# Kernel optimization log

Hardware: AMD Instinct MI355X
Metric: run time of the kernel (lower is better)

## Reference

```python
import jax, jax.numpy as jnp
import numpy as np

N = 16384      # total nodes
E = 262144     # edges (avg degree 16)
HID = 1024     # hidden_dim
D = 768        # internal_dim
R = 6          # num_relations
B = 4          # num_bases
L = 2          # num_gnn_layers
BN_EPS = 1e-5
LN_EPS = 1e-5


def setup_inputs() -> dict:
    key = jax.random.key(0)
    ks = jax.random.split(key, 16)
    s = 0.02
    return {
        "h_text": jax.random.normal(ks[0], (N, HID), jnp.float32),
        "edge_index": jax.random.randint(ks[1], (2, E), 0, N, jnp.int32),
        "edge_type": jax.random.randint(ks[2], (E,), 0, R, jnp.int32),
        # input projection
        "w_in": jax.random.normal(ks[3], (HID, D), jnp.float32) * s,
        "b_in": jnp.zeros((D,), jnp.float32),
        # per-layer RGCN params (stacked over L layers)
        "basis": jax.random.normal(ks[4], (L, B, D, D), jnp.float32) * s,
        "comp": jax.random.normal(ks[5], (L, R, B), jnp.float32),
        "root": jax.random.normal(ks[6], (L, D, D), jnp.float32) * s,
        "conv_bias": jnp.zeros((L, D), jnp.float32),
        # per-layer BatchNorm affine params
        "bn_gamma": jnp.ones((L, D), jnp.float32),
        "bn_beta": jnp.zeros((L, D), jnp.float32),
        # output projection + LayerNorm
        "w_out": jax.random.normal(ks[7], (D, HID), jnp.float32) * s,
        "b_out": jnp.zeros((HID,), jnp.float32),
        "ln_gamma": jnp.ones((HID,), jnp.float32),
        "ln_beta": jnp.zeros((HID,), jnp.float32),
    }


def _rgcn_conv(x, src, dst, edge_type, basis, comp, root, bias):
    """PyG RGCNConv with basis decomposition, per-relation mean aggregation."""
    n = x.shape[0]
    # relation weights: W_r = sum_b comp[r,b] * basis[b]  -> [R, D, D]
    W = jnp.einsum('rb,bio->rio', comp, basis)
    # transform every node by every relation once: [R, N, D]
    h_all = jnp.einsum('ni,rio->rno', x, W)
    # per-(relation, target) in-degree for mean normalization
    counts = jnp.zeros((R, n), x.dtype).at[edge_type, dst].add(1.0)
    norm = 1.0 / counts[edge_type, dst]            # each indexed count >= 1
    msg = h_all[edge_type, src] * norm[:, None]    # [E, D] gathered messages
    agg = jax.ops.segment_sum(msg, dst, num_segments=n)
    return agg + x @ root + bias


def _batchnorm(x, gamma, beta):
    mean = jnp.mean(x, axis=0)
    var = jnp.var(x, axis=0)  # biased, as in torch BN training forward
    return gamma * (x - mean) * jax.lax.rsqrt(var + BN_EPS) + beta


def _layernorm(x, gamma, beta):
    mean = jnp.mean(x, axis=-1, keepdims=True)
    var = jnp.var(x, axis=-1, keepdims=True)
    return gamma * (x - mean) * jax.lax.rsqrt(var + LN_EPS) + beta


def reference(h_text, edge_index, edge_type, w_in, b_in, basis, comp, root,
              conv_bias, bn_gamma, bn_beta, w_out, b_out, ln_gamma, ln_beta):
    src, dst = edge_index[0], edge_index[1]
    x = jax.nn.relu(h_text @ w_in + b_in)
    for l in range(L):
        h_in = x
        x = _rgcn_conv(x, src, dst, edge_type, basis[l], comp[l], root[l], conv_bias[l])
        x = jax.nn.relu(x)
        x = x + h_in
        x = _batchnorm(x, bn_gamma[l], bn_beta[l])
    h_final = x @ w_out + b_out
    return _layernorm(h_final, ln_gamma, ln_beta)
```

## Files before the change

kernel.cpp:

```cpp
#include <hip/hip_runtime.h>
#include <hip/hip_bf16.h>

#define NN 16384
#define NE 262144
#define HIDD 1024
#define DD 768
#define RR 6
#define BB 4
#define LL 2
#define BN_EPS 1e-5f
#define LN_EPS 1e-5f

typedef __attribute__((ext_vector_type(8))) short bf16x8;
typedef __attribute__((ext_vector_type(4))) float f32x4;

__device__ __forceinline__ float b2f(unsigned short u) {
  union { unsigned int i; float f; } c;
  c.i = ((unsigned int)u) << 16;
  return c.f;
}
__device__ __forceinline__ unsigned short f2b(float f) {
  union { float f; unsigned int u; } c;
  c.f = f;
  unsigned int x = c.u;
  x += 0x7FFFu + ((x >> 16) & 1u);
  return (unsigned short)(x >> 16);
}

__device__ __forceinline__ void gll16(const unsigned short* g, unsigned short* l) {
  __builtin_amdgcn_global_load_lds(
      (const __attribute__((address_space(1))) unsigned int*)g,
      (__attribute__((address_space(3))) unsigned int*)l, 16, 0, 0);
}

__global__ void k_detect(const unsigned short* __restrict__ h, int* __restrict__ flag) {
  __shared__ int sh[256];
  int cnt = 0;
  for (int k = 0; k < 256; ++k) {
    ushort4 t = *(const ushort4*)&h[(size_t)(k * 256 + threadIdx.x) * 4];
    if ((t.x & 0x7F80) == 0x7F80) cnt++;
    if ((t.y & 0x7F80) == 0x7F80) cnt++;
    if ((t.z & 0x7F80) == 0x7F80) cnt++;
    if ((t.w & 0x7F80) == 0x7F80) cnt++;
  }
  sh[threadIdx.x] = cnt;
  __syncthreads();
  if (threadIdx.x == 0) {
    int t = 0;
    for (int i = 0; i < 256; ++i) t += sh[i];
    flag[0] = (t > 16) ? 1 : 0;
  }
}

template <int MODE>
__device__ __forceinline__ float load1t(const void* p, size_t i, int isf32) {
  if (MODE == 1 || (MODE == 0 && isf32)) return ((const float*)p)[i];
  return b2f(((const unsigned short*)p)[i]);
}

__global__ void k_cvt8(const void* s0, const void* s1, const void* s2, const void* s3,
                       const void* s4, const void* s5, const void* s6, const void* s7,
                       float* __restrict__ fpar, const int* __restrict__ flagp) {
  const int isf32 = flagp[0];
  const int seg = blockIdx.y;
  const int lens[8] = {768, 48, 1536, 1536, 1536, 1024, 1024, 1024};
  const int offs_[8] = {0, 768, 816, 2352, 3888, 5424, 6448, 7472};
  const void* srcs[8] = {s0, s1, s2, s3, s4, s5, s6, s7};
  int i = blockIdx.x * 256 + threadIdx.x;
  if (i < lens[seg]) fpar[offs_[seg] + i] = load1t<0>(srcs[seg], i, isf32);
}

__global__ void k_cvtb(const void* __restrict__ in, unsigned short* __restrict__ out,
                       int n, const int* __restrict__ flagp) {
  const int isf32 = flagp[0];
  int i = blockIdx.x * 256 + threadIdx.x;
  if (i < n) out[i] = f2b(load1t<0>(in, (size_t)i, isf32));
}

__global__ void k_fill(float* __restrict__ out, long n, float val) {
  long i = (long)blockIdx.x * 256 + threadIdx.x;
  if (i < n) out[i] = val;
}

__global__ __launch_bounds__(256) void k_transpose(const void* __restrict__ src,
                                                   long ioff,
                                                   unsigned short* __restrict__ dst,
                                                   int I, int J, int dstStride,
                                                   int dstOff,
                                                   const int* __restrict__ flagp) {
  const int isf32 = flagp[0];
  __shared__ unsigned short t[64][65];
  const int j0 = blockIdx.x * 64, i0 = blockIdx.y * 64;
  const int tx = threadIdx.x & 63, ty = threadIdx.x >> 6;
  for (int rr = ty; rr < 64; rr += 4)
    t[rr][tx] = f2b(load1t<0>(src, (size_t)ioff + (size_t)(i0 + rr) * J + j0 + tx, isf32));
  __syncthreads();
  for (int rr = ty; rr < 64; rr += 4)
    dst[(size_t)(j0 + rr) * dstStride + dstOff + i0 + tx] = t[tx][rr];
}

__global__ __launch_bounds__(256) void k_tbatch(const void* __restrict__ root, long roff,
                                                const void* __restrict__ basis, long boff,
                                                unsigned short* __restrict__ BT,
                                                const int* __restrict__ flagp) {
  const int isf32 = flagp[0];
  const int z = blockIdx.z;
  const void* src = (z == 0) ? root : basis;
  const long off = (z == 0) ? roff : boff + (long)(z - 1) * DD * DD;
  __shared__ unsigned short t[64][65];
  const int j0 = blockIdx.x * 64, i0 = blockIdx.y * 64;
  const int tx = threadIdx.x & 63, ty = threadIdx.x >> 6;
  for (int rr = ty; rr < 64; rr += 4)
    t[rr][tx] = f2b(load1t<0>(src, (size_t)off + (size_t)(i0 + rr) * DD + j0 + tx, isf32));
  __syncthreads();
  for (int rr = ty; rr < 64; rr += 4)
    BT[(size_t)(j0 + rr) * (5 * DD) + z * DD + i0 + tx] = t[tx][rr];
}

template <int BIAS, int RELU, int OUTB>
__global__ __launch_bounds__(256) void k_mgemm(const unsigned short* __restrict__ A,
                                               const unsigned short* __restrict__ Bt,
                                               const float* __restrict__ bias,
                                               void* __restrict__ C,
                                               int M, int Nn, int K) {
  __shared__ __align__(16) unsigned short Alds[2][128 * 32];
  __shared__ __align__(16) unsigned short Blds[2][128 * 32];
  const int tid = threadIdx.x;
  const int lane = tid & 63, w = tid >> 6;
  const int wm = w >> 1, wn = w & 1;
  const int fr = lane & 15, kg = lane >> 4;
  const int nwg = gridDim.x;
  int id = blockIdx.x;
  if ((nwg & 7) == 0) id = (id & 7) * (nwg >> 3) + (id >> 3);
  const int gx = Nn >> 7;
  const int m0 = (id / gx) * 128, n0 = (id % gx) * 128;

  const int srow = w * 16 + (lane >> 2);
  const int sslot = (lane & 3) ^ ((lane >> 3) & 3);
  const unsigned short* ga = A + (size_t)(m0 + srow) * K + sslot * 8;
  const unsigned short* ga2 = ga + (size_t)64 * K;
  const unsigned short* gb = Bt + (size_t)(n0 + srow) * K + sslot * 8;
  const unsigned short* gb2 = gb + (size_t)64 * K;
  const int wo = w * 512;
  const int roff = fr * 32 + ((kg ^ ((fr >> 1) & 3)) * 8);

  f32x4 acc[4][4] = {};

  for (int k0 = 0; k0 < K; k0 += 64) {
    gll16(ga + k0, &Alds[0][wo]);
    gll16(ga2 + k0, &Alds[0][wo + 2048]);
    gll16(gb + k0, &Blds[0][wo]);
    gll16(gb2 + k0, &Blds[0][wo + 2048]);
    gll16(ga + k0 + 32, &Alds[1][wo]);
    gll16(ga2 + k0 + 32, &Alds[1][wo + 2048]);
    gll16(gb + k0 + 32, &Blds[1][wo]);
    gll16(gb2 + k0 + 32, &Blds[1][wo + 2048]);
    __syncthreads();
#pragma unroll
    for (int kh = 0; kh < 2; ++kh) {
      bf16x8 af[4], bfr[4];
#pragma unroll
      for (int i = 0; i < 4; ++i) {
        af[i] = *(const bf16x8*)(&Alds[kh][(wm * 4 + i) * 512 + roff]);
        bfr[i] = *(const bf16x8*)(&Blds[kh][(wn * 4 + i) * 512 + roff]);
      }
#pragma unroll
      for (int i = 0; i < 4; ++i)
#pragma unroll
        for (int j = 0; j < 4; ++j)
          acc[i][j] = __builtin_amdgcn_mfma_f32_16x16x32_bf16(af[i], bfr[j],
                                                              acc[i][j], 0, 0, 0);
    }
    __syncthreads();
  }

  const int orow = (lane >> 4) * 4;
#pragma unroll
  for (int i = 0; i < 4; ++i) {
#pragma unroll
    for (int j = 0; j < 4; ++j) {
      const int n = n0 + wn * 64 + j * 16 + fr;
      const float bv = BIAS ? bias[n] : 0.f;
#pragma unroll
      for (int rg = 0; rg < 4; ++rg) {
        const int m = m0 + wm * 64 + i * 16 + orow + rg;
        const size_t off = (size_t)m * Nn + n;
        float v = acc[i][j][rg] + bv;
        if (RELU) v = fmaxf(v, 0.f);
        if (OUTB) ((unsigned short*)C)[off] = f2b(v);
        else      ((float*)C)[off] = v;
      }
    }
  }
}

__global__ __launch_bounds__(256) void k_mgemm3(const unsigned short* __restrict__ x0,
                                                const unsigned short* __restrict__ Y01,
                                                const unsigned short* __restrict__ Y23,
                                                const unsigned short* __restrict__ BT,
                                                const float* __restrict__ cbias,
                                                unsigned short* __restrict__ yb,
                                                float* __restrict__ sums,
                                                float* __restrict__ sqs) {
  __shared__ __align__(16) unsigned short Alds[2][128 * 32];
  __shared__ __align__(16) unsigned short Blds[2][128 * 32];
  __shared__ float csum[128], csq[128];
  const int tid = threadIdx.x;
  const int lane = tid & 63, w = tid >> 6;
  const int wm = w >> 1, wn = w & 1;
  const int fr = lane & 15, kg = lane >> 4;
  const int nwg = gridDim.x;
  int id = blockIdx.x;
  id = (id & 7) * (nwg >> 3) + (id >> 3);
  const int m0 = (id / 6) * 128, n0 = (id % 6) * 128;

  const int srow = w * 16 + (lane >> 2);
  const int sslot = (lane & 3) ^ ((lane >> 3) & 3);
  const unsigned short* gxp = x0 + (size_t)(m0 + srow) * DD + sslot * 8;
  const unsigned short* gxp2 = gxp + (size_t)64 * DD;
  const unsigned short* gy = Y01 + (size_t)(m0 + srow) * 1536 + sslot * 8;
  const unsigned short* gy2 = gy + (size_t)64 * 1536;
  const unsigned short* gz = Y23 + (size_t)(m0 + srow) * 1536 + sslot * 8;
  const unsigned short* gz2 = gz + (size_t)64 * 1536;
  const unsigned short* gb = BT + (size_t)(n0 + srow) * 3840 + sslot * 8;
  const unsigned short* gb2 = gb + (size_t)64 * 3840;
  const int wo = w * 512;
  const int roff = fr * 32 + ((kg ^ ((fr >> 1) & 3)) * 8);

  f32x4 acc[4][4] = {};

  for (int k0 = 0; k0 < 3840; k0 += 64) {
    const unsigned short *pa, *pa2;
    long ko;
    if (k0 < 768)       { pa = gxp; pa2 = gxp2; ko = k0; }
    else if (k0 < 2304) { pa = gy;  pa2 = gy2;  ko = k0 - 768; }
    else                { pa = gz;  pa2 = gz2;  ko = k0 - 2304; }
    gll16(pa + ko, &Alds[0][wo]);
    gll16(pa2 + ko, &Alds[0][wo + 2048]);
    gll16(pa + ko + 32, &Alds[1][wo]);
    gll16(pa2 + ko + 32, &Alds[1][wo + 2048]);
    gll16(gb + k0, &Blds[0][wo]);
    gll16(gb2 + k0, &Blds[0][wo + 2048]);
    gll16(gb + k0 + 32, &Blds[1][wo]);
    gll16(gb2 + k0 + 32, &Blds[1][wo + 2048]);
    __syncthreads();
#pragma unroll
    for (int kh = 0; kh < 2; ++kh) {
      bf16x8 af[4], bfr[4];
#pragma unroll
      for (int i = 0; i < 4; ++i) {
        af[i] = *(const bf16x8*)(&Alds[kh][(wm * 4 + i) * 512 + roff]);
        bfr[i] = *(const bf16x8*)(&Blds[kh][(wn * 4 + i) * 512 + roff]);
      }
#pragma unroll
      for (int i = 0; i < 4; ++i)
#pragma unroll
        for (int j = 0; j < 4; ++j)
          acc[i][j] = __builtin_amdgcn_mfma_f32_16x16x32_bf16(af[i], bfr[j],
                                                              acc[i][j], 0, 0, 0);
    }
    __syncthreads();
  }

  if (tid < 128) { csum[tid] = 0.f; csq[tid] = 0.f; }
  __syncthreads();
  const int orow = (lane >> 4) * 4;
#pragma unroll
  for (int j = 0; j < 4; ++j) {
    const int nloc = wn * 64 + j * 16 + fr;
    const int n = n0 + nloc;
    const float cb = cbias[n];
    float ps = 0.f, pq = 0.f;
#pragma unroll
    for (int i = 0; i < 4; ++i) {
#pragma unroll
      for (int rg = 0; rg < 4; ++rg) {
        const int m = m0 + wm * 64 + i * 16 + orow + rg;
        float v = fmaxf(acc[i][j][rg] + cb, 0.f) + b2f(x0[(size_t)m * DD + n]);
        yb[(size_t)m * DD + n] = f2b(v);
        ps += v;
        pq += v * v;
      }
    }
    atomicAdd(&csum[nloc], ps);
    atomicAdd(&csq[nloc], pq);
  }
  __syncthreads();
  if (tid < 128) {
    atomicAdd(&sums[n0 + tid], csum[tid]);
    atomicAdd(&sqs[n0 + tid], csq[tid]);
  }
}

__global__ void k_count(const int* __restrict__ et, const int* __restrict__ dst,
                        float* __restrict__ counts) {
  int e = blockIdx.x * 256 + threadIdx.x;
  if (e < NE) atomicAdd(&counts[(size_t)et[e] * NN + dst[e]], 1.0f);
}

__global__ void k_deg(const int* __restrict__ dst, int* __restrict__ deg) {
  int e = blockIdx.x * 256 + threadIdx.x;
  if (e < NE) atomicAdd(&deg[dst[e]], 1);
}

__global__ __launch_bounds__(256) void k_scan(const int* __restrict__ deg,
                                              int* __restrict__ offs,
                                              int* __restrict__ cursor) {
  __shared__ int part[256];
  const int base = threadIdx.x * 64;
  int s = 0;
  for (int i = 0; i < 64; ++i) s += deg[base + i];
  part[threadIdx.x] = s;
  __syncthreads();
  if (threadIdx.x == 0) {
    int run = 0;
    for (int i = 0; i < 256; ++i) { int t = part[i]; part[i] = run; run += t; }
  }
  __syncthreads();
  int run = part[threadIdx.x];
  for (int i = 0; i < 64; ++i) {
    offs[base + i] = run;
    cursor[base + i] = run;
    run += deg[base + i];
  }
  if (threadIdx.x == 255) offs[NN] = run;
}

__global__ void k_place(const int* __restrict__ src, const int* __restrict__ dst,
                        const int* __restrict__ et, int* __restrict__ cursor,
                        int* __restrict__ elist) {
  int e = blockIdx.x * 256 + threadIdx.x;
  if (e >= NE) return;
  int d = dst[e];
  int slot = atomicAdd(&cursor[d], 1);
  elist[slot] = src[e] | (et[e] << 20);
}

__global__ __launch_bounds__(192) void k_gather4(const int* __restrict__ offs,
                                                 const int* __restrict__ elist,
                                                 const float* __restrict__ counts,
                                                 const float* __restrict__ compL,
                                                 const unsigned short* __restrict__ x0,
                                                 unsigned short* __restrict__ Y01,
                                                 unsigned short* __restrict__ Y23) {
  const int d = blockIdx.x;
  const int tid = threadIdx.x;
  __shared__ float sw[RR][4];
  if (tid < 4 * RR) {
    const int r = tid >> 2, j = tid & 3;
    const float c = counts[(size_t)r * NN + d];
    sw[r][j] = (c > 0.f) ? compL[r * BB + j] / c : 0.f;
  }
  __syncthreads();
  const int beg = offs[d], end = offs[d + 1];
  float a0[4] = {}, a1[4] = {}, a2[4] = {}, a3[4] = {};
  int e = beg;
  for (; e + 3 < end; e += 4) {
    const int v1 = elist[e], v2 = elist[e + 1], v3 = elist[e + 2], v4 = elist[e + 3];
    const int s1 = v1 & 0xFFFFF, r1 = v1 >> 20;
    const int s2 = v2 & 0xFFFFF, r2 = v2 >> 20;
    const int s3 = v3 & 0xFFFFF, r3 = v3 >> 20;
    const int s4 = v4 & 0xFFFFF, r4 = v4 >> 20;
    ushort4 t1 = *(const ushort4*)&x0[(size_t)s1 * DD + tid * 4];
    ushort4 t2 = *(const ushort4*)&x0[(size_t)s2 * DD + tid * 4];
    ushort4 t3 = *(const ushort4*)&x0[(size_t)s3 * DD + tid * 4];
    ushort4 t4 = *(const ushort4*)&x0[(size_t)s4 * DD + tid * 4];
    const float f1[4] = {b2f(t1.x), b2f(t1.y), b2f(t1.z), b2f(t1.w)};
    const float f2[4] = {b2f(t2.x), b2f(t2.y), b2f(t2.z), b2f(t2.w)};
    const float f3[4] = {b2f(t3.x), b2f(t3.y), b2f(t3.z), b2f(t3.w)};
    const float f4[4] = {b2f(t4.x), b2f(t4.y), b2f(t4.z), b2f(t4.w)};
#pragma unroll
    for (int c = 0; c < 4; ++c) {
      a0[c] += sw[r1][0] * f1[c] + sw[r2][0] * f2[c] + sw[r3][0] * f3[c] + sw[r4][0] * f4[c];
      a1[c] += sw[r1][1] * f1[c] + sw[r2][1] * f2[c] + sw[r3][1] * f3[c] + sw[r4][1] * f4[c];
      a2[c] += sw[r1][2] * f1[c] + sw[r2][2] * f2[c] + sw[r3][2] * f3[c] + sw[r4][2] * f4[c];
      a3[c] += sw[r1][3] * f1[c] + sw[r2][3] * f2[c] + sw[r3][3] * f3[c] + sw[r4][3] * f4[c];
    }
  }
  for (; e < end; ++e) {
    const int v = elist[e];
    const int s = v & 0xFFFFF, r = v >> 20;
    ushort4 t = *(const ushort4*)&x0[(size_t)s * DD + tid * 4];
    const float f[4] = {b2f(t.x), b2f(t.y), b2f(t.z), b2f(t.w)};
#pragma unroll
    for (int c = 0; c < 4; ++c) {
      a0[c] += sw[r][0] * f[c];
      a1[c] += sw[r][1] * f[c];
      a2[c] += sw[r][2] * f[c];
      a3[c] += sw[r][3] * f[c];
    }
  }
  ushort4 o;
  o.x = f2b(a0[0]); o.y = f2b(a0[1]); o.z = f2b(a0[2]); o.w = f2b(a0[3]);
  *(ushort4*)&Y01[(size_t)d * 1536 + tid * 4] = o;
  o.x = f2b(a1[0]); o.y = f2b(a1[1]); o.z = f2b(a1[2]); o.w = f2b(a1[3]);
  *(ushort4*)&Y01[(size_t)d * 1536 + DD + tid * 4] = o;
  o.x = f2b(a2[0]); o.y = f2b(a2[1]); o.z = f2b(a2[2]); o.w = f2b(a2[3]);
  *(ushort4*)&Y23[(size_t)d * 1536 + tid * 4] = o;
  o.x = f2b(a3[0]); o.y = f2b(a3[1]); o.z = f2b(a3[2]); o.w = f2b(a3[3]);
  *(ushort4*)&Y23[(size_t)d * 1536 + DD + tid * 4] = o;
}

__global__ void k_bn_apply(const unsigned short* __restrict__ yb,
                           const float* __restrict__ gamma,
                           const float* __restrict__ beta,
                           const float* __restrict__ sums,
                           const float* __restrict__ sqs,
                           unsigned short* __restrict__ xout) {
  size_t idx = (size_t)blockIdx.x * 256 + threadIdx.x;
  if (idx >= (size_t)NN * DD) return;
  int c = idx % DD;
  float mu = sums[c] * (1.0f / NN);
  float var = sqs[c] * (1.0f / NN) - mu * mu;
  xout[idx] = f2b(gamma[c] * (b2f(yb[idx]) - mu) * rsqrtf(var + BN_EPS) + beta[c]);
}

__global__ __launch_bounds__(256) void k_layernorm(const float* __restrict__ hf,
                                                   const float* __restrict__ gamma,
                                                   const float* __restrict__ beta,
                                                   float* __restrict__ out) {
  const int row = blockIdx.x;
  const float* h = hf + (size_t)row * HIDD;
  float v[4];
  float s = 0.f, sq = 0.f;
#pragma unroll
  for (int j = 0; j < 4; ++j) {
    v[j] = h[threadIdx.x + j * 256];
    s += v[j];
    sq += v[j] * v[j];
  }
#pragma unroll
  for (int off = 32; off > 0; off >>= 1) {
    s += __shfl_down(s, off);
    sq += __shfl_down(sq, off);
  }
  __shared__ float ps[4], pq[4];
  const int lane = threadIdx.x & 63, wv = threadIdx.x >> 6;
  if (lane == 0) { ps[wv] = s; pq[wv] = sq; }
  __syncthreads();
  if (threadIdx.x == 0) {
    float ts = ps[0] + ps[1] + ps[2] + ps[3];
    float tq = pq[0] + pq[1] + pq[2] + pq[3];
    float mu = ts * (1.0f / HIDD);
    float var = tq * (1.0f / HIDD) - mu * mu;
    ps[0] = mu;
    pq[0] = rsqrtf(var + LN_EPS);
  }
  __syncthreads();
  const float mu = ps[0], rstd = pq[0];
#pragma unroll
  for (int j = 0; j < 4; ++j) {
    const int c = threadIdx.x + j * 256;
    out[(size_t)row * HIDD + c] = gamma[c] * (v[j] - mu) * rstd + beta[c];
  }
}

extern "C" void kernel_launch(void* const* d_in, const int* in_sizes, int n_in,
                              void* d_out, int out_size, void* d_ws, size_t ws_size,
                              hipStream_t stream) {
  const void* h_text = d_in[0];
  const int* ei      = (const int*)d_in[1];
  const int* etype   = (const int*)d_in[2];
  const void* w_in  = d_in[3];
  const void* b_in  = d_in[4];
  const void* basis = d_in[5];
  const void* comp  = d_in[6];
  const void* root  = d_in[7];
  const void* convb = d_in[8];
  const void* bn_g  = d_in[9];
  const void* bn_b  = d_in[10];
  const void* w_out = d_in[11];
  const void* b_out = d_in[12];
  const void* ln_g  = d_in[13];
  const void* ln_b  = d_in[14];
  float* out = (float*)d_out;

  const int* src = ei;
  const int* dst = ei + NE;

  char* W = (char*)d_ws;
  int*   flags  = (int*)(W + 0);
  float* stats  = (float*)(W + 256);
  float* fpar   = (float*)(W + 6400);
  float* f_bin  = fpar;
  float* f_comp = fpar + 768;
  float* f_cb   = fpar + 816;
  float* f_bng  = fpar + 2352;
  float* f_bnb  = fpar + 3888;
  float* f_bout = fpar + 5424;
  float* f_lng  = fpar + 6448;
  float* f_lnb  = fpar + 7472;
  float* counts = (float*)(W + 40384);
  int*   deg    = (int*)(W + 433600);
  int*   offs   = (int*)(W + 499136);
  int*   cursor = (int*)(W + 564736);
  int*   elist  = (int*)(W + 630272);
  unsigned short* BTcat = (unsigned short*)(W + 1678848);
  unsigned short* x0    = (unsigned short*)(W + 7577088);
  unsigned short* Y23   = (unsigned short*)(W + 32742912);
  unsigned short* yb_ws = (unsigned short*)(W + 83074560);
  const size_t NEED_B = 133406208;
  if (ws_size < NEED_B) {
    k_fill<<<(int)(((long)out_size + 255) / 256), 256, 0, stream>>>(
        out, (long)out_size, (float)(ws_size >> 20) * 100.0f);
    return;
  }

  unsigned short* h16   = (unsigned short*)d_out;
  unsigned short* wt_in = (unsigned short*)d_out + 29360128;
  unsigned short* Y01   = (unsigned short*)d_out;
  float* hf = out;
  unsigned short* wt_out = BTcat;

  k_detect<<<1, 256, 0, stream>>>((const unsigned short*)h_text, flags);
  {
    dim3 g(6, 8);
    k_cvt8<<<g, 256, 0, stream>>>(b_in, comp, convb, bn_g, bn_b, b_out, ln_g,
                                  ln_b, fpar, flags);
  }

  k_cvtb<<<(NN * HIDD) / 256, 256, 0, stream>>>(h_text, h16, NN * HIDD, flags);
  {
    dim3 g(DD / 64, HIDD / 64);
    k_transpose<<<g, 256, 0, stream>>>(w_in, 0, wt_in, HIDD, DD, HIDD, 0, flags);
  }

  k_mgemm<1, 1, 1><<<(DD / 128) * (NN / 128), 256, 0, stream>>>(
      h16, wt_in, f_bin, x0, NN, DD, HIDD);

  hipMemsetAsync(counts, 0, (size_t)RR * NN * sizeof(float), stream);
  k_count<<<NE / 256, 256, 0, stream>>>(etype, dst, counts);
  hipMemsetAsync(deg, 0, NN * sizeof(int), stream);
  k_deg<<<NE / 256, 256, 0, stream>>>(dst, deg);
  k_scan<<<1, 256, 0, stream>>>(deg, offs, cursor);
  k_place<<<NE / 256, 256, 0, stream>>>(src, dst, etype, cursor, elist);

  for (int l = 0; l < LL; ++l) {
    const long boff = (long)l * BB * DD * DD;
    const long roff = (long)l * DD * DD;
    const float* compL = f_comp + l * RR * BB;
    const float* cbL   = f_cb + l * DD;
    const float* gL    = f_bng + l * DD;
    const float* bL    = f_bnb + l * DD;

    k_gather4<<<NN, 192, 0, stream>>>(offs, elist, counts, compL, x0, Y01, Y23);
    {
      dim3 g(DD / 64, DD / 64, 5);
      k_tbatch<<<g, 256, 0, stream>>>(root, roff, basis, boff, BTcat, flags);
    }
    hipMemsetAsync(stats, 0, 2 * DD * sizeof(float), stream);
    k_mgemm3<<<(DD / 128) * (NN / 128), 256, 0, stream>>>(
        x0, Y01, Y23, BTcat, cbL, yb_ws, stats, stats + DD);
    k_bn_apply<<<(int)(((size_t)NN * DD + 255) / 256), 256, 0, stream>>>(
        yb_ws, gL, bL, stats, stats + DD, x0);
  }

  {
    dim3 g(HIDD / 64, DD / 64);
    k_transpose<<<g, 256, 0, stream>>>(w_out, 0, wt_out, DD, HIDD, DD, 0, flags);
  }
  k_mgemm<1, 0, 0><<<(HIDD / 128) * (NN / 128), 256, 0, stream>>>(
      x0, wt_out, f_bout, hf, NN, HIDD, DD);

  k_layernorm<<<NN, 256, 0, stream>>>(hf, f_lng, f_lnb, out);
}
```

Baseline: 750.6 us.

## Fold BatchNorm affine into downstream gather, GEMM weights and biases

```diff
diff --git a/kernel.cpp b/kernel.cpp
--- a/kernel.cpp
+++ b/kernel.cpp
@@ -87,13 +87,16 @@
                                                    unsigned short* __restrict__ dst,
                                                    int I, int J, int dstStride,
                                                    int dstOff,
+                                                   const float* __restrict__ rowsc,
                                                    const int* __restrict__ flagp) {
   const int isf32 = flagp[0];
   __shared__ unsigned short t[64][65];
   const int j0 = blockIdx.x * 64, i0 = blockIdx.y * 64;
   const int tx = threadIdx.x & 63, ty = threadIdx.x >> 6;
-  for (int rr = ty; rr < 64; rr += 4)
-    t[rr][tx] = f2b(load1t<0>(src, (size_t)ioff + (size_t)(i0 + rr) * J + j0 + tx, isf32));
+  for (int rr = ty; rr < 64; rr += 4) {
+    float sc = rowsc ? rowsc[i0 + rr] : 1.0f;
+    t[rr][tx] = f2b(sc * load1t<0>(src, (size_t)ioff + (size_t)(i0 + rr) * J + j0 + tx, isf32));
+  }
   __syncthreads();
   for (int rr = ty; rr < 64; rr += 4)
     dst[(size_t)(j0 + rr) * dstStride + dstOff + i0 + tx] = t[tx][rr];
@@ -101,6 +104,7 @@
 
 __global__ __launch_bounds__(256) void k_tbatch(const void* __restrict__ root, long roff,
                                                 const void* __restrict__ basis, long boff,
+                                                const float* __restrict__ grho,
                                                 unsigned short* __restrict__ BT,
                                                 const int* __restrict__ flagp) {
   const int isf32 = flagp[0];
@@ -110,11 +114,44 @@
   __shared__ unsigned short t[64][65];
   const int j0 = blockIdx.x * 64, i0 = blockIdx.y * 64;
   const int tx = threadIdx.x & 63, ty = threadIdx.x >> 6;
-  for (int rr = ty; rr < 64; rr += 4)
-    t[rr][tx] = f2b(load1t<0>(src, (size_t)off + (size_t)(i0 + rr) * DD + j0 + tx, isf32));
+  for (int rr = ty; rr < 64; rr += 4) {
+    float sc = (z == 0) ? grho[i0 + rr] : 1.0f;
+    t[rr][tx] = f2b(sc * load1t<0>(src, (size_t)off + (size_t)(i0 + rr) * DD + j0 + tx, isf32));
+  }
   __syncthreads();
   for (int rr = ty; rr < 64; rr += 4)
     BT[(size_t)(j0 + rr) * (5 * DD) + z * DD + i0 + tx] = t[tx][rr];
+}
+
+__global__ void k_affinit(float* __restrict__ grho, float* __restrict__ dlt) {
+  int i = blockIdx.x * 256 + threadIdx.x;
+  if (i < DD) { grho[i] = 1.0f; dlt[i] = 0.0f; }
+}
+
+__global__ void k_aff(const float* __restrict__ sums, const float* __restrict__ sqs,
+                      const float* __restrict__ gamma, const float* __restrict__ beta,
+                      float* __restrict__ grho, float* __restrict__ dlt) {
+  int c = blockIdx.x * 256 + threadIdx.x;
+  if (c >= DD) return;
+  float mu = sums[c] * (1.0f / NN);
+  float var = sqs[c] * (1.0f / NN) - mu * mu;
+  float gr = gamma[c] * rsqrtf(var + BN_EPS);
+  grho[c] = gr;
+  dlt[c] = beta[c] - gr * mu;
+}
+
+__global__ void k_rowbias(const void* __restrict__ mat, long ioff, int J,
+                          const float* __restrict__ delta,
+                          const float* __restrict__ base,
+                          float* __restrict__ outb,
+                          const int* __restrict__ flagp) {
+  const int isf32 = flagp[0];
+  int n = blockIdx.x * 256 + threadIdx.x;
+  if (n >= J) return;
+  float s = base ? base[n] : 0.0f;
+  for (int k = 0; k < DD; ++k)
+    s += delta[k] * load1t<0>(mat, (size_t)ioff + (size_t)k * J + n, isf32);
+  outb[n] = s;
 }
 
 template <int BIAS, int RELU, int OUTB>
@@ -194,12 +231,14 @@
   }
 }
 
-__global__ __launch_bounds__(256) void k_mgemm3(const unsigned short* __restrict__ x0,
+__global__ __launch_bounds__(256) void k_mgemm3(const unsigned short* __restrict__ ybprev,
                                                 const unsigned short* __restrict__ Y01,
                                                 const unsigned short* __restrict__ Y23,
                                                 const unsigned short* __restrict__ BT,
-                                                const float* __restrict__ cbias,
-                                                unsigned short* __restrict__ yb,
+                                                const float* __restrict__ rbias,
+                                                const float* __restrict__ grho,
+                                                const float* __restrict__ dlt,
+                                                unsigned short* __restrict__ ybnew,
                                                 float* __restrict__ sums,
                                                 float* __restrict__ sqs) {
   __shared__ __align__(16) unsigned short Alds[2][128 * 32];
@@ -216,7 +255,7 @@
 
   const int srow = w * 16 + (lane >> 2);
   const int sslot = (lane & 3) ^ ((lane >> 3) & 3);
-  const unsigned short* gxp = x0 + (size_t)(m0 + srow) * DD + sslot * 8;
+  const unsigned short* gxp = ybprev + (size_t)(m0 + srow) * DD + sslot * 8;
   const unsigned short* gxp2 = gxp + (size_t)64 * DD;
   const unsigned short* gy = Y01 + (size_t)(m0 + srow) * 1536 + sslot * 8;
   const unsigned short* gy2 = gy + (size_t)64 * 1536;
@@ -269,15 +308,17 @@
   for (int j = 0; j < 4; ++j) {
     const int nloc = wn * 64 + j * 16 + fr;
     const int n = n0 + nloc;
-    const float cb = cbias[n];
+    const float rb = rbias[n];
+    const float gr = grho[n], dl = dlt[n];
     float ps = 0.f, pq = 0.f;
 #pragma unroll
     for (int i = 0; i < 4; ++i) {
 #pragma unroll
       for (int rg = 0; rg < 4; ++rg) {
         const int m = m0 + wm * 64 + i * 16 + orow + rg;
-        float v = fmaxf(acc[i][j][rg] + cb, 0.f) + b2f(x0[(size_t)m * DD + n]);
-        yb[(size_t)m * DD + n] = f2b(v);
+        float xin = gr * b2f(ybprev[(size_t)m * DD + n]) + dl;
+        float v = fmaxf(acc[i][j][rg] + rb, 0.f) + xin;
+        ybnew[(size_t)m * DD + n] = f2b(v);
         ps += v;
         pq += v * v;
       }
@@ -340,7 +381,9 @@
                                                  const int* __restrict__ elist,
                                                  const float* __restrict__ counts,
                                                  const float* __restrict__ compL,
-                                                 const unsigned short* __restrict__ x0,
+                                                 const float* __restrict__ grho,
+                                                 const float* __restrict__ dlt,
+                                                 const unsigned short* __restrict__ yb,
                                                  unsigned short* __restrict__ Y01,
                                                  unsigned short* __restrict__ Y23) {
   const int d = blockIdx.x;
@@ -354,65 +397,71 @@
   __syncthreads();
   const int beg = offs[d], end = offs[d + 1];
   float a0[4] = {}, a1[4] = {}, a2[4] = {}, a3[4] = {};
+  float ws0 = 0.f, ws1 = 0.f, ws2 = 0.f, ws3 = 0.f;
   int e = beg;
-  for (; e + 3 < end; e += 4) {
-    const int v1 = elist[e], v2 = elist[e + 1], v3 = elist[e + 2], v4 = elist[e + 3];
-    const int s1 = v1 & 0xFFFFF, r1 = v1 >> 20;
-    const int s2 = v2 & 0xFFFFF, r2 = v2 >> 20;
-    const int s3 = v3 & 0xFFFFF, r3 = v3 >> 20;
-    const int s4 = v4 & 0xFFFFF, r4 = v4 >> 20;
-    ushort4 t1 = *(const ushort4*)&x0[(size_t)s1 * DD + tid * 4];
-    ushort4 t2 = *(const ushort4*)&x0[(size_t)s2 * DD + tid * 4];
-    ushort4 t3 = *(const ushort4*)&x0[(size_t)s3 * DD + tid * 4];
-    ushort4 t4 = *(const ushort4*)&x0[(size_t)s4 * DD + tid * 4];
-    const float f1[4] = {b2f(t1.x), b2f(t1.y), b2f(t1.z), b2f(t1.w)};
-    const float f2[4] = {b2f(t2.x), b2f(t2.y), b2f(t2.z), b2f(t2.w)};
-    const float f3[4] = {b2f(t3.x), b2f(t3.y), b2f(t3.z), b2f(t3.w)};
-    const float f4[4] = {b2f(t4.x), b2f(t4.y), b2f(t4.z), b2f(t4.w)};
-#pragma unroll
-    for (int c = 0; c < 4; ++c) {
-      a0[c] += sw[r1][0] * f1[c] + sw[r2][0] * f2[c] + sw[r3][0] * f3[c] + sw[r4][0] * f4[c];
-      a1[c] += sw[r1][1] * f1[c] + sw[r2][1] * f2[c] + sw[r3][1] * f3[c] + sw[r4][1] * f4[c];
-      a2[c] += sw[r1][2] * f1[c] + sw[r2][2] * f2[c] + sw[r3][2] * f3[c] + sw[r4][2] * f4[c];
-      a3[c] += sw[r1][3] * f1[c] + sw[r2][3] * f2[c] + sw[r3][3] * f3[c] + sw[r4][3] * f4[c];
+  for (; e + 7 < end; e += 8) {
+    int v[8];
+#pragma unroll
+    for (int q = 0; q < 8; ++q) v[q] = elist[e + q];
+    ushort4 t[8];
+#pragma unroll
+    for (int q = 0; q < 8; ++q)
+      t[q] = *(const ushort4*)&yb[(size_t)(v[q] & 0xFFFFF) * DD + tid * 4];
+#pragma unroll
+    for (int q = 0; q < 8; ++q) {
+      const int r = v[q] >> 20;
+      const float w0 = sw[r][0], w1 = sw[r][1], w2 = sw[r][2], w3 = sw[r][3];
+      ws0 += w0; ws1 += w1; ws2 += w2; ws3 += w3;
+      const float f[4] = {b2f(t[q].x), b2f(t[q].y), b2f(t[q].z), b2f(t[q].w)};
+#pragma unroll
+      for (int c = 0; c < 4; ++c) {
+        a0[c] += w0 * f[c];
+        a1[c] += w1 * f[c];
+        a2[c] += w2 * f[c];
+        a3[c] += w3 * f[c];
+      }
     }
   }
   for (; e < end; ++e) {
     const int v = elist[e];
     const int s = v & 0xFFFFF, r = v >> 20;
-    ushort4 t = *(const ushort4*)&x0[(size_t)s * DD + tid * 4];
+    ushort4 t = *(const ushort4*)&yb[(size_t)s * DD + tid * 4];
+    const float w0 = sw[r][0], w1 = sw[r][1], w2 = sw[r][2], w3 = sw[r][3];
+    ws0 += w0; ws1 += w1; ws2 += w2; ws3 += w3;
     const float f[4] = {b2f(t.x), b2f(t.y), b2f(t.z), b2f(t.w)};
 #pragma unroll
     for (int c = 0; c < 4; ++c) {
-      a0[c] += sw[r][0] * f[c];
-      a1[c] += sw[r][1] * f[c];
-      a2[c] += sw[r][2] * f[c];
-      a3[c] += sw[r][3] * f[c];
+      a0[c] += w0 * f[c];
+      a1[c] += w1 * f[c];
+      a2[c] += w2 * f[c];
+      a3[c] += w3 * f[c];
     }
   }
+  const float4 gr = *(const float4*)&grho[tid * 4];
+  const float4 dl = *(const float4*)&dlt[tid * 4];
+  const float grv[4] = {gr.x, gr.y, gr.z, gr.w};
+  const float dlv[4] = {dl.x, dl.y, dl.z, dl.w};
   ushort4 o;
-  o.x = f2b(a0[0]); o.y = f2b(a0[1]); o.z = f2b(a0[2]); o.w = f2b(a0[3]);
+  o.x = f2b(grv[0] * a0[0] + dlv[0] * ws0);
+  o.y = f2b(grv[1] * a0[1] + dlv[1] * ws0);
+  o.z = f2b(grv[2] * a0[2] + dlv[2] * ws0);
+  o.w = f2b(grv[3] * a0[3] + dlv[3] * ws0);
   *(ushort4*)&Y01[(size_t)d * 1536 + tid * 4] = o;
-  o.x = f2b(a1[0]); o.y = f2b(a1[1]); o.z = f2b(a1[2]); o.w = f2b(a1[3]);
+  o.x = f2b(grv[0] * a1[0] + dlv[0] * ws1);
+  o.y = f2b(grv[1] * a1[1] + dlv[1] * ws1);
+  o.z = f2b(grv[2] * a1[2] + dlv[2] * ws1);
+  o.w = f2b(grv[3] * a1[3] + dlv[3] * ws1);
   *(ushort4*)&Y01[(size_t)d * 1536 + DD + tid * 4] = o;
-  o.x = f2b(a2[0]); o.y = f2b(a2[1]); o.z = f2b(a2[2]); o.w = f2b(a2[3]);
+  o.x = f2b(grv[0] * a2[0] + dlv[0] * ws2);
+  o.y = f2b(grv[1] * a2[1] + dlv[1] * ws2);
+  o.z = f2b(grv[2] * a2[2] + dlv[2] * ws2);
+  o.w = f2b(grv[3] * a2[3] + dlv[3] * ws2);
   *(ushort4*)&Y23[(size_t)d * 1536 + tid * 4] = o;
-  o.x = f2b(a3[0]); o.y = f2b(a3[1]); o.z = f2b(a3[2]); o.w = f2b(a3[3]);
+  o.x = f2b(grv[0] * a3[0] + dlv[0] * ws3);
+  o.y = f2b(grv[1] * a3[1] + dlv[1] * ws3);
+  o.z = f2b(grv[2] * a3[2] + dlv[2] * ws3);
+  o.w = f2b(grv[3] * a3[3] + dlv[3] * ws3);
   *(ushort4*)&Y23[(size_t)d * 1536 + DD + tid * 4] = o;
-}
-
-__global__ void k_bn_apply(const unsigned short* __restrict__ yb,
-                           const float* __restrict__ gamma,
-                           const float* __restrict__ beta,
-                           const float* __restrict__ sums,
-                           const float* __restrict__ sqs,
-                           unsigned short* __restrict__ xout) {
-  size_t idx = (size_t)blockIdx.x * 256 + threadIdx.x;
-  if (idx >= (size_t)NN * DD) return;
-  int c = idx % DD;
-  float mu = sums[c] * (1.0f / NN);
-  float var = sqs[c] * (1.0f / NN) - mu * mu;
-  xout[idx] = f2b(gamma[c] * (b2f(yb[idx]) - mu) * rsqrtf(var + BN_EPS) + beta[c]);
 }
 
 __global__ __launch_bounds__(256) void k_layernorm(const float* __restrict__ hf,
@@ -490,16 +539,22 @@
   float* f_bout = fpar + 5424;
   float* f_lng  = fpar + 6448;
   float* f_lnb  = fpar + 7472;
-  float* counts = (float*)(W + 40384);
-  int*   deg    = (int*)(W + 433600);
-  int*   offs   = (int*)(W + 499136);
-  int*   cursor = (int*)(W + 564736);
-  int*   elist  = (int*)(W + 630272);
-  unsigned short* BTcat = (unsigned short*)(W + 1678848);
-  unsigned short* x0    = (unsigned short*)(W + 7577088);
-  unsigned short* Y23   = (unsigned short*)(W + 32742912);
-  unsigned short* yb_ws = (unsigned short*)(W + 83074560);
-  const size_t NEED_B = 133406208;
+  float* affA_g = (float*)(W + 40384);
+  float* affA_d = affA_g + DD;
+  float* affB_g = (float*)(W + 46528);
+  float* affB_d = affB_g + DD;
+  float* rbias  = (float*)(W + 52672);
+  float* bobias = (float*)(W + 55744);
+  float* counts = (float*)(W + 59840);
+  int*   deg    = (int*)(W + 453056);
+  int*   offs   = (int*)(W + 518592);
+  int*   cursor = (int*)(W + 584192);
+  int*   elist  = (int*)(W + 649728);
+  unsigned short* BTcat = (unsigned short*)(W + 1698304);
+  unsigned short* yb0   = (unsigned short*)(W + 7596544);
+  unsigned short* Y23   = (unsigned short*)(W + 32762368);
+  unsigned short* yb1   = (unsigned short*)(W + 83094016);
+  const size_t NEED_B = 108259840;
   if (ws_size < NEED_B) {
     k_fill<<<(int)(((long)out_size + 255) / 256), 256, 0, stream>>>(
         out, (long)out_size, (float)(ws_size >> 20) * 100.0f);
@@ -522,11 +577,12 @@
   k_cvtb<<<(NN * HIDD) / 256, 256, 0, stream>>>(h_text, h16, NN * HIDD, flags);
   {
     dim3 g(DD / 64, HIDD / 64);
-    k_transpose<<<g, 256, 0, stream>>>(w_in, 0, wt_in, HIDD, DD, HIDD, 0, flags);
+    k_transpose<<<g, 256, 0, stream>>>(w_in, 0, wt_in, HIDD, DD, HIDD, 0,
+                                       nullptr, flags);
   }
 
   k_mgemm<1, 1, 1><<<(DD / 128) * (NN / 128), 256, 0, stream>>>(
-      h16, wt_in, f_bin, x0, NN, DD, HIDD);
+      h16, wt_in, f_bin, yb0, NN, DD, HIDD);
 
   hipMemsetAsync(counts, 0, (size_t)RR * NN * sizeof(float), stream);
   k_count<<<NE / 256, 256, 0, stream>>>(etype, dst, counts);
@@ -534,6 +590,7 @@
   k_deg<<<NE / 256, 256, 0, stream>>>(dst, deg);
   k_scan<<<1, 256, 0, stream>>>(deg, offs, cursor);
   k_place<<<NE / 256, 256, 0, stream>>>(src, dst, etype, cursor, elist);
+  k_affinit<<<3, 256, 0, stream>>>(affA_g, affA_d);
 
   for (int l = 0; l < LL; ++l) {
     const long boff = (long)l * BB * DD * DD;
@@ -542,25 +599,34 @@
     const float* cbL   = f_cb + l * DD;
     const float* gL    = f_bng + l * DD;
     const float* bL    = f_bnb + l * DD;
-
-    k_gather4<<<NN, 192, 0, stream>>>(offs, elist, counts, compL, x0, Y01, Y23);
+    const float* aff_g = (l == 0) ? affA_g : affB_g;
+    const float* aff_d = (l == 0) ? affA_d : affB_d;
+    float* affo_g = (l == 0) ? affB_g : affA_g;
+    float* affo_d = (l == 0) ? affB_d : affA_d;
+    const unsigned short* ybin = (l == 0) ? yb0 : yb1;
+    unsigned short* ybout      = (l == 0) ? yb1 : yb0;
+
+    k_rowbias<<<3, 256, 0, stream>>>(root, roff, DD, aff_d, cbL, rbias, flags);
     {
       dim3 g(DD / 64, DD / 64, 5);
-      k_tbatch<<<g, 256, 0, stream>>>(root, roff, basis, boff, BTcat, flags);
+      k_tbatch<<<g, 256, 0, stream>>>(root, roff, basis, boff, aff_g, BTcat, flags);
     }
+    k_gather4<<<NN, 192, 0, stream>>>(offs, elist, counts, compL, aff_g, aff_d,
+                                      ybin, Y01, Y23);
     hipMemsetAsync(stats, 0, 2 * DD * sizeof(float), stream);
     k_mgemm3<<<(DD / 128) * (NN / 128), 256, 0, stream>>>(
-        x0, Y01, Y23, BTcat, cbL, yb_ws, stats, stats + DD);
-    k_bn_apply<<<(int)(((size_t)NN * DD + 255) / 256), 256, 0, stream>>>(
-        yb_ws, gL, bL, stats, stats + DD, x0);
-  }
-
+        ybin, Y01, Y23, BTcat, rbias, aff_g, aff_d, ybout, stats, stats + DD);
+    k_aff<<<3, 256, 0, stream>>>(stats, stats + DD, gL, bL, affo_g, affo_d);
+  }
+
+  k_rowbias<<<4, 256, 0, stream>>>(w_out, 0, HIDD, affA_d, f_bout, bobias, flags);
   {
     dim3 g(HIDD / 64, DD / 64);
-    k_transpose<<<g, 256, 0, stream>>>(w_out, 0, wt_out, DD, HIDD, DD, 0, flags);
+    k_transpose<<<g, 256, 0, stream>>>(w_out, 0, wt_out, DD, HIDD, DD, 0,
+                                       affA_g, flags);
   }
   k_mgemm<1, 0, 0><<<(HIDD / 128) * (NN / 128), 256, 0, stream>>>(
-      x0, wt_out, f_bout, hf, NN, HIDD, DD);
+      yb0, wt_out, bobias, hf, NN, HIDD, DD);
 
   k_layernorm<<<NN, 256, 0, stream>>>(hf, f_lng, f_lnb, out);
 }
```

Measured after the change: 979.3 us. 30.5% more time.
